# Optimization experiments

Measured on AMD Instinct MI355X. Metric: run time of the kernel, lower is better.

The kernel has to match this reference:

```python
import jax, jax.numpy as jnp
import numpy as np

# Complete 4-ary tree, leaves at depth 8, heap layout (children of i are 4i+1..4i+4).
B_ARY = 4
DEPTH = 8          # depths 0..8, leaves at depth 8
H = 512            # hidden_channels
IN = 512           # in_channels
OUT = 256          # out_channels
L = 2              # num_layers
LEVEL_STARTS = np.array([(B_ARY ** d - 1) // (B_ARY - 1) for d in range(DEPTH + 2)])
N = int(LEVEL_STARTS[-1])  # 87381


def setup_inputs() -> dict:
    key = jax.random.key(0)
    ks = jax.random.split(key, 12)
    x = jax.random.normal(ks[0], (N, IN), jnp.float32)

    # tree structure (numpy, deterministic)
    n_internal = int(LEVEL_STARTS[DEPTH])
    child_idx = np.zeros((N, B_ARY), np.int32)
    child_mask = np.zeros((N, B_ARY), np.int32)
    internal = np.arange(n_internal)
    child_idx[:n_internal] = (internal[:, None] * B_ARY + 1 + np.arange(B_ARY)[None, :]).astype(np.int32)
    child_mask[:n_internal] = 1
    node_parent = np.full(N, -1, np.int64)
    node_parent[1:] = (np.arange(1, N) - 1) // B_ARY
    node_depth = np.zeros(N, np.int64)
    for d in range(DEPTH + 1):
        node_depth[LEVEL_STARTS[d]:LEVEL_STARTS[d + 1]] = d
    is_leaf = node_depth == DEPTH
    edge_index = np.stack([np.arange(1, N), node_parent[1:]]).astype(np.int64)
    batch = np.zeros(N, np.int64)

    s = 0.02
    params = dict(
        W_in=jax.random.normal(ks[1], (IN, H), jnp.float32) * s,
        b_in=jnp.zeros((H,), jnp.float32),
        W_ioux=jax.random.normal(ks[2], (L, H, 3 * H), jnp.float32) * s,
        b_ioux=jnp.zeros((L, 3 * H), jnp.float32),
        W_iouh=jax.random.normal(ks[3], (L, H, 3 * H), jnp.float32) * s,
        b_iouh=jnp.zeros((L, 3 * H), jnp.float32),
        W_fx=jax.random.normal(ks[4], (L, H, H), jnp.float32) * s,
        b_fx=jnp.zeros((L, H), jnp.float32),
        W_fh=jax.random.normal(ks[5], (L, H, H), jnp.float32) * s,
        b_fh=jnp.zeros((L, H), jnp.float32),
        W_out=jax.random.normal(ks[6], (H, OUT), jnp.float32) * s,
        b_out=jnp.zeros((OUT,), jnp.float32),
    )
    return dict(
        x=x,
        edge_index=jnp.asarray(edge_index),
        batch=jnp.asarray(batch),
        node_depth=jnp.asarray(node_depth),
        node_parent=jnp.asarray(node_parent),
        is_leaf=jnp.asarray(is_leaf),
        child_idx=jnp.asarray(child_idx),
        child_mask=jnp.asarray(child_mask),
        **params,
    )


def reference(x, edge_index, batch, node_depth, node_parent, is_leaf,
              child_idx, child_mask,
              W_in, b_in, W_ioux, b_ioux, W_iouh, b_iouh,
              W_fx, b_fx, W_fh, b_fh, W_out, b_out):
    cm = child_mask.astype(x.dtype)  # [N, B]
    h = jax.nn.relu(x @ W_in + b_in)  # input projection (dropout = eval mode identity)
    for l in range(L):
        hidden = jnp.zeros((N, H), x.dtype)
        cell = jnp.zeros((N, H), x.dtype)
        # bottom-up over tree levels; levels are contiguous static slices
        for d in range(DEPTH, -1, -1):
            s, e = int(LEVEL_STARTS[d]), int(LEVEL_STARTS[d + 1])
            xl = h[s:e]                                   # [n_d, H]
            ci = child_idx[s:e]                           # [n_d, B]
            m = cm[s:e][..., None]                        # [n_d, B, 1]
            ch = hidden[ci] * m                           # masked child hidden
            cc = cell[ci] * m                             # masked child cell
            h_sum = ch.sum(axis=1)                        # child-sum
            iou = xl @ W_ioux[l] + b_ioux[l] + h_sum @ W_iouh[l] + b_iouh[l]
            i, o, u = jnp.split(iou, 3, axis=-1)
            i = jax.nn.sigmoid(i)
            o = jax.nn.sigmoid(o)
            u = jnp.tanh(u)
            f = jax.nn.sigmoid((xl @ W_fx[l] + b_fx[l])[:, None, :] + ch @ W_fh[l] + b_fh[l])
            c = i * u + (f * cc).sum(axis=1)
            hl = o * jnp.tanh(c)
            hidden = hidden.at[s:e].set(hl)
            cell = cell.at[s:e].set(c)
        h = hidden
    node_emb = h @ W_out + b_out                          # [N, OUT]
    tree_emb = jax.ops.segment_sum(node_emb, batch, num_segments=1)  # 'sum' aggregation
    return node_emb, tree_emb
```

## Files before the change

### kernel.cpp

```cpp
#include <hip/hip_runtime.h>

typedef __bf16 bf16;
typedef __bf16 bf16x8 __attribute__((ext_vector_type(8)));
typedef float f32x4 __attribute__((ext_vector_type(4)));

#define NN 87381
#define NINT 21845
#define NLEAF 65536
#define LEAF_START 21845

__device__ __forceinline__ float sigmoidf_(float x) {
    return 1.0f / (1.0f + __expf(-x));
}
__device__ __forceinline__ float tanhf_(float x) {
    return 1.0f - 2.0f / (__expf(2.0f * x) + 1.0f);
}

__device__ __forceinline__ void gload_lds16(const bf16* g, bf16* l) {
    __builtin_amdgcn_global_load_lds(
        (const __attribute__((address_space(1))) unsigned int*)g,
        (__attribute__((address_space(3))) unsigned int*)l, 16, 0, 0);
}

__device__ __forceinline__ int xcd_swz(int bid, int nwg) {
    int q = nwg >> 3, r = nwg & 7;
    int x = bid & 7, i = bid >> 3;
    return (x < r ? x * (q + 1) : r * (q + 1) + (x - r) * q) + i;
}

#define SWZ(r, kc) ((((r) << 3) | ((kc) ^ ((r) & 7))) << 3)

__global__ void tconv_kernel(const float* __restrict__ W, bf16* __restrict__ Wt,
                             int NR, int total) {
    int idx = blockIdx.x * 256 + threadIdx.x;
    if (idx >= total) return;
    int n = idx >> 9;
    int k = idx & 511;
    Wt[idx] = (bf16)W[(size_t)k * NR + n];
}

__global__ void tcat_kernel(const float* __restrict__ W1, const float* __restrict__ W2,
                            bf16* __restrict__ Wt, int NR, int total) {
    int idx = blockIdx.x * 256 + threadIdx.x;
    if (idx >= total) return;
    int n = idx >> 10;
    int kk = idx & 1023;
    const float* src = (kk < 512) ? W1 : W2;
    int k = kk & 511;
    Wt[idx] = (bf16)src[(size_t)k * NR + n];
}

__global__ void convx_kernel(const float* __restrict__ X, bf16* __restrict__ Y, int total4) {
    int idx = blockIdx.x * 256 + threadIdx.x;
    if (idx >= total4) return;
    const float4 f = *reinterpret_cast<const float4*>(X + (size_t)idx * 4);
    bf16 o[4] = {(bf16)f.x, (bf16)f.y, (bf16)f.z, (bf16)f.w};
    *reinterpret_cast<ushort2*>(Y + (size_t)idx * 4 + 0) = *reinterpret_cast<ushort2*>(&o[0]);
    *reinterpret_cast<ushort2*>(Y + (size_t)idx * 4 + 2) = *reinterpret_cast<ushort2*>(&o[2]);
}

__global__ void hs_kernel(const bf16* __restrict__ hc, bf16* __restrict__ hs, int total8)
{
    int idx = blockIdx.x * 256 + threadIdx.x;
    if (idx >= total8) return;
    int p  = idx >> 6;
    int j0 = (idx & 63) << 3;
    const bf16* base = hc + ((size_t)(4 * p) << 9) + j0;
    float a8[8];
#pragma unroll
    for (int t = 0; t < 8; ++t) a8[t] = 0.f;
#pragma unroll
    for (int k = 0; k < 4; ++k) {
        const bf16x8 v = *reinterpret_cast<const bf16x8*>(base + (k << 9));
#pragma unroll
        for (int t = 0; t < 8; ++t) a8[t] += (float)v[t];
    }
    bf16x8 o;
#pragma unroll
    for (int t = 0; t < 8; ++t) o[t] = (bf16)a8[t];
    *reinterpret_cast<bf16x8*>(&hs[(size_t)idx * 8]) = o;
}

#define MFMA_COMPUTE_2x4(As, Bs, acc, wm, wn, lm, quad)                          \
    _Pragma("unroll")                                                            \
    for (int kk = 0; kk < 64; kk += 32) {                                        \
        const int kc_ = (kk >> 3) + quad;                                        \
        bf16x8 areg[2], breg[4];                                                 \
        _Pragma("unroll")                                                        \
        for (int mi = 0; mi < 2; ++mi)                                           \
            areg[mi] = *reinterpret_cast<const bf16x8*>(                         \
                &(As)[SWZ(wm + mi * 16 + lm, kc_)]);                             \
        _Pragma("unroll")                                                        \
        for (int ni = 0; ni < 4; ++ni)                                           \
            breg[ni] = *reinterpret_cast<const bf16x8*>(                         \
                &(Bs)[SWZ(wn + ni * 16 + lm, kc_)]);                             \
        _Pragma("unroll")                                                        \
        for (int mi = 0; mi < 2; ++mi)                                           \
            _Pragma("unroll")                                                    \
            for (int ni = 0; ni < 4; ++ni)                                       \
                acc[mi][ni] = __builtin_amdgcn_mfma_f32_16x16x32_bf16(           \
                    areg[mi], breg[ni], acc[mi][ni], 0, 0, 0);                   \
    }

__global__ __launch_bounds__(512)
void gemm_kernel(const bf16* __restrict__ A, const bf16* __restrict__ Bt,
                 int bstride, int K, int ntiles,
                 float* __restrict__ Cf, bf16* __restrict__ Cb,
                 const float* __restrict__ bias1, const float* __restrict__ bias2,
                 int M, int N, int relu, int swz)
{
    __shared__ __align__(16) bf16 As[2][128 * 64];
    __shared__ __align__(16) bf16 Bs[2][128 * 64];
    const int tid  = threadIdx.x;
    const int wave = tid >> 6;
    const int lane = tid & 63;
    int bid = blockIdx.x;
    if (swz) bid = xcd_swz(bid, (int)gridDim.x);
    const int bm = (bid / ntiles) * 128;
    const int bn = (bid % ntiles) * 128;
    const int wm = (wave & 3) * 32;
    const int wn = (wave >> 2) * 64;
    const int lm   = lane & 15;
    const int quad = lane >> 4;

    f32x4 acc[2][4];
#pragma unroll
    for (int i = 0; i < 2; ++i)
#pragma unroll
        for (int j = 0; j < 4; ++j) acc[i][j] = (f32x4){0.f, 0.f, 0.f, 0.f};

    auto stage = [&](int buf, int k0) {
#pragma unroll
        for (int i = 0; i < 2; ++i) {
            int c   = i * 512 + tid;
            int r   = c >> 3;
            int kc8 = ((c & 7) ^ (r & 7)) << 3;
            int gr  = bm + r; gr = (gr < M) ? gr : (M - 1);
            gload_lds16(A + (size_t)gr * K + k0 + kc8, &As[buf][c << 3]);
        }
#pragma unroll
        for (int i = 0; i < 2; ++i) {
            int c   = i * 512 + tid;
            int r   = c >> 3;
            int kc8 = ((c & 7) ^ (r & 7)) << 3;
            gload_lds16(Bt + (size_t)(bn + r) * bstride + k0 + kc8, &Bs[buf][c << 3]);
        }
    };

    const int nk = K >> 6;
    stage(0, 0);
    __syncthreads();
    int cur = 0;
    for (int t = 0; t < nk; ++t) {
        if (t + 1 < nk) stage(cur ^ 1, (t + 1) << 6);
        MFMA_COMPUTE_2x4(As[cur], Bs[cur], acc, wm, wn, lm, quad);
        __syncthreads();
        cur ^= 1;
    }

#pragma unroll
    for (int ni = 0; ni < 4; ++ni) {
        int col = bn + wn + ni * 16 + lm;
        float bsum = (bias1 ? bias1[col] : 0.f) + (bias2 ? bias2[col] : 0.f);
#pragma unroll
        for (int mi = 0; mi < 2; ++mi) {
#pragma unroll
            for (int r = 0; r < 4; ++r) {
                int row = bm + wm + mi * 16 + quad * 4 + r;
                if (row < M) {
                    float v = acc[mi][ni][r] + bsum;
                    if (relu) v = (v > 0.f) ? v : 0.f;
                    if (Cf) Cf[(size_t)row * N + col] = v;
                    else    Cb[(size_t)row * N + col] = (bf16)v;
                }
            }
        }
    }
}

__global__ __launch_bounds__(512)
void iou_fused_kernel(const bf16* __restrict__ A0, const bf16* __restrict__ A1,
                      int K, const bf16* __restrict__ wiou,
                      const float* __restrict__ bx1, const float* __restrict__ bx2,
                      const float* __restrict__ fcs,
                      bf16* __restrict__ hout, float* __restrict__ cellout,
                      int M, int swz)
{
    __shared__ __align__(16) bf16 As[2][128 * 64];
    __shared__ __align__(16) bf16 Bs[2][3 * 64 * 64];
    const int tid  = threadIdx.x;
    const int wave = tid >> 6;
    const int lane = tid & 63;
    int bid = blockIdx.x;
    if (swz) bid = xcd_swz(bid, (int)gridDim.x);
    const int bm = (bid >> 3) * 128;
    const int bn = (bid & 7) * 64;
    if (bm >= M) return;
    const int wm   = (wave & 3) * 32;
    const int wn   = (wave >> 2) * 32;
    const int lm   = lane & 15;
    const int quad = lane >> 4;

    f32x4 acc[3][2][2];
#pragma unroll
    for (int g = 0; g < 3; ++g)
#pragma unroll
        for (int i = 0; i < 2; ++i)
#pragma unroll
            for (int j = 0; j < 2; ++j) acc[g][i][j] = (f32x4){0.f, 0.f, 0.f, 0.f};

    auto stage = [&](int buf, int k0) {
        const bf16* Aseg = (k0 < 512) ? A0 : A1;
        const int kseg0 = k0 & 511;
#pragma unroll
        for (int i = 0; i < 2; ++i) {
            int c   = i * 512 + tid;
            int r   = c >> 3;
            int kc8 = ((c & 7) ^ (r & 7)) << 3;
            int gr  = bm + r; gr = (gr < M) ? gr : (M - 1);
            gload_lds16(Aseg + ((size_t)gr << 9) + kseg0 + kc8, &As[buf][c << 3]);
        }
#pragma unroll
        for (int i = 0; i < 3; ++i) {
            int c   = i * 512 + tid;
            int g   = c >> 9;
            int cg  = c & 511;
            int r   = cg >> 3;
            int kc8 = ((cg & 7) ^ (r & 7)) << 3;
            gload_lds16(wiou + (size_t)(g * 512 + bn + r) * 1024 + k0 + kc8,
                        &Bs[buf][c << 3]);
        }
    };

    const int nk = K >> 6;
    stage(0, 0);
    __syncthreads();
    int cur = 0;
    for (int t = 0; t < nk; ++t) {
        if (t + 1 < nk) stage(cur ^ 1, (t + 1) << 6);
#pragma unroll
        for (int kk = 0; kk < 64; kk += 32) {
            const int kc_ = (kk >> 3) + quad;
            bf16x8 areg[2];
#pragma unroll
            for (int mi = 0; mi < 2; ++mi)
                areg[mi] = *reinterpret_cast<const bf16x8*>(
                    &As[cur][SWZ(wm + mi * 16 + lm, kc_)]);
            bf16x8 breg[3][2];
#pragma unroll
            for (int g = 0; g < 3; ++g)
#pragma unroll
                for (int ni = 0; ni < 2; ++ni)
                    breg[g][ni] = *reinterpret_cast<const bf16x8*>(
                        &Bs[cur][g * 4096 + SWZ(wn + ni * 16 + lm, kc_)]);
#pragma unroll
            for (int g = 0; g < 3; ++g)
#pragma unroll
                for (int mi = 0; mi < 2; ++mi)
#pragma unroll
                    for (int ni = 0; ni < 2; ++ni)
                        acc[g][mi][ni] = __builtin_amdgcn_mfma_f32_16x16x32_bf16(
                            areg[mi], breg[g][ni], acc[g][mi][ni], 0, 0, 0);
        }
        __syncthreads();
        cur ^= 1;
    }

#pragma unroll
    for (int ni = 0; ni < 2; ++ni) {
        int col = bn + wn + ni * 16 + lm;
        float bi = bx1[col]        + bx2[col];
        float bo = bx1[col + 512]  + bx2[col + 512];
        float bu = bx1[col + 1024] + bx2[col + 1024];
#pragma unroll
        for (int mi = 0; mi < 2; ++mi) {
#pragma unroll
            for (int r = 0; r < 4; ++r) {
                int row = bm + wm + mi * 16 + quad * 4 + r;
                if (row < M) {
                    float i_ = sigmoidf_(acc[0][mi][ni][r] + bi);
                    float o_ = sigmoidf_(acc[1][mi][ni][r] + bo);
                    float u_ = tanhf_(acc[2][mi][ni][r] + bu);
                    float c  = i_ * u_ + (fcs ? fcs[(size_t)row * 512 + col] : 0.f);
                    cellout[(size_t)row * 512 + col] = c;
                    hout[(size_t)row * 512 + col] = (bf16)(o_ * tanhf_(c));
                }
            }
        }
    }
}

__global__ __launch_bounds__(512)
void cf_kernel(const bf16* __restrict__ hp, const bf16* __restrict__ hc,
               const float* __restrict__ cellc, const bf16* __restrict__ wf,
               const float* __restrict__ bf1, const float* __restrict__ bf2,
               float* __restrict__ fcs, int E, int swz)
{
    const int M = 4 * E;
    __shared__ __align__(16) bf16 As[2][128 * 64];
    __shared__ __align__(16) bf16 Bs[2][128 * 64];
    const int tid  = threadIdx.x;
    const int wave = tid >> 6;
    const int lane = tid & 63;
    int bid = blockIdx.x;
    if (swz) bid = xcd_swz(bid, (int)gridDim.x);
    const int bm = (bid >> 2) * 128;
    const int bn = (bid & 3) * 128;
    if (bm >= M) return;
    const int wm   = (wave & 3) * 32;
    const int wn   = (wave >> 2) * 64;
    const int lm   = lane & 15;
    const int quad = lane >> 4;

    f32x4 acc[2][4];
#pragma unroll
    for (int i = 0; i < 2; ++i)
#pragma unroll
        for (int j = 0; j < 4; ++j) acc[i][j] = (f32x4){0.f, 0.f, 0.f, 0.f};

    auto stage = [&](int buf, int k0) {
        const int seg   = k0 >> 9;
        const int kseg0 = k0 & 511;
#pragma unroll
        for (int i = 0; i < 2; ++i) {
            int c   = i * 512 + tid;
            int r   = c >> 3;
            int kc8 = ((c & 7) ^ (r & 7)) << 3;
            int gr  = bm + r; gr = (gr < M) ? gr : (M - 1);
            const bf16* src = (seg == 0) ? (hp + ((size_t)(gr >> 2) << 9))
                                         : (hc + ((size_t)gr << 9));
            gload_lds16(src + kseg0 + kc8, &As[buf][c << 3]);
        }
#pragma unroll
        for (int i = 0; i < 2; ++i) {
            int c   = i * 512 + tid;
            int r   = c >> 3;
            int kc8 = ((c & 7) ^ (r & 7)) << 3;
            gload_lds16(wf + (size_t)(bn + r) * 1024 + k0 + kc8, &Bs[buf][c << 3]);
        }
    };

    stage(0, 0);
    __syncthreads();
    int cur = 0;
    for (int t = 0; t < 16; ++t) {
        if (t + 1 < 16) stage(cur ^ 1, (t + 1) << 6);
        MFMA_COMPUTE_2x4(As[cur], Bs[cur], acc, wm, wn, lm, quad);
        __syncthreads();
        cur ^= 1;
    }

#pragma unroll
    for (int ni = 0; ni < 4; ++ni) {
        int col = bn + wn + ni * 16 + lm;
        float bsum = bf1[col] + bf2[col];
#pragma unroll
        for (int mi = 0; mi < 2; ++mi) {
            int R0 = bm + wm + mi * 16;
            if (R0 + quad * 4 < M) {
                float fc = 0.f;
#pragma unroll
                for (int r = 0; r < 4; ++r) {
                    int row = R0 + quad * 4 + r;
                    fc += sigmoidf_(acc[mi][ni][r] + bsum) *
                          cellc[(size_t)row * 512 + col];
                }
                fcs[(size_t)((R0 >> 2) + quad) * 512 + col] = fc;
            }
        }
    }
}

#define R1_BLOCKS 2048
#define R1_ROWS 43
__global__ void reduce1_kernel(const float* __restrict__ ne, float* __restrict__ partial)
{
    int t = threadIdx.x;
    int b = blockIdx.x;
    int r0 = b * R1_ROWS;
    int r1 = r0 + R1_ROWS; r1 = (r1 < NN) ? r1 : NN;
    float acc = 0.f;
    for (int r = r0; r < r1; ++r) acc += ne[(size_t)r * 256 + t];
    partial[(size_t)b * 256 + t] = acc;
}
__global__ void reduce2_kernel(const float* __restrict__ partial, float* __restrict__ partial2)
{
    int t = threadIdx.x;
    int b = blockIdx.x;
    float acc = 0.f;
    for (int i = 0; i < 32; ++i) acc += partial[(size_t)(b * 32 + i) * 256 + t];
    partial2[(size_t)b * 256 + t] = acc;
}
__global__ void reduce3_kernel(const float* __restrict__ partial2, float* __restrict__ tree)
{
    int t = threadIdx.x;
    float acc = 0.f;
    for (int i = 0; i < 64; ++i) acc += partial2[(size_t)i * 256 + t];
    tree[t] = acc;
}

extern "C" void kernel_launch(void* const* d_in, const int* in_sizes, int n_in,
                              void* d_out, int out_size, void* d_ws, size_t ws_size,
                              hipStream_t stream)
{
    const float* x      = (const float*)d_in[0];
    const float* W_in   = (const float*)d_in[8];
    const float* b_in   = (const float*)d_in[9];
    const float* W_ioux = (const float*)d_in[10];
    const float* b_ioux = (const float*)d_in[11];
    const float* W_iouh = (const float*)d_in[12];
    const float* b_iouh = (const float*)d_in[13];
    const float* W_fx   = (const float*)d_in[14];
    const float* b_fx   = (const float*)d_in[15];
    const float* W_fh   = (const float*)d_in[16];
    const float* b_fh   = (const float*)d_in[17];
    const float* W_out  = (const float*)d_in[18];
    const float* b_out  = (const float*)d_in[19];

    static const int LS[10] = {0, 1, 5, 21, 85, 341, 1365, 5461, 21845, 87381};

    char* ws = (char*)d_ws;
    size_t off = 0;
    auto take = [&](size_t bytes) -> void* {
        void* p = ws + off;
        off += (bytes + 255) & ~(size_t)255;
        return p;
    };
    bf16*  wt_in      = (bf16*) take((size_t)512 * 512 * 2);
    bf16*  wt_out     = (bf16*) take((size_t)256 * 512 * 2);
    bf16*  wt_iou_cat = (bf16*) take((size_t)2 * 1536 * 1024 * 2);
    bf16*  wt_f_cat   = (bf16*) take((size_t)2 * 512 * 1024 * 2);
    bf16*  h          = (bf16*) take((size_t)NN * 512 * 2);
    bf16*  hint1      = (bf16*) take((size_t)NINT * 512 * 2);
    bf16*  hB         = (bf16*) take((size_t)NLEAF * 512 * 2);
    float* cell_int   = (float*)take((size_t)NINT * 512 * 4);
    float* cell_leaf  = (float*)take((size_t)NLEAF * 512 * 4);
    float* fcsum      = (float*)take((size_t)16384 * 512 * 4);
    bf16*  hsbuf      = (bf16*) take((size_t)16384 * 512 * 2);
    float* partial    = (float*)take((size_t)R1_BLOCKS * 256 * 4);
    float* partial2   = (float*)take((size_t)64 * 256 * 4);
    bf16*  xbf        = (bf16*)cell_leaf;

    dim3 blk(256), blk512(512);
    auto tgrid = [](int total) { return dim3((unsigned)((total + 255) / 256)); };

    tconv_kernel<<<tgrid(512 * 512), blk, 0, stream>>>(W_in, wt_in, 512, 512 * 512);
    tconv_kernel<<<tgrid(256 * 512), blk, 0, stream>>>(W_out, wt_out, 256, 256 * 512);
    for (int l = 0; l < 2; ++l) {
        tcat_kernel<<<tgrid(1536 * 1024), blk, 0, stream>>>(
            W_ioux + (size_t)l * 512 * 1536, W_iouh + (size_t)l * 512 * 1536,
            wt_iou_cat + (size_t)l * 1536 * 1024, 1536, 1536 * 1024);
        tcat_kernel<<<tgrid(512 * 1024), blk, 0, stream>>>(
            W_fx + (size_t)l * 512 * 512, W_fh + (size_t)l * 512 * 512,
            wt_f_cat + (size_t)l * 512 * 1024, 512, 512 * 1024);
    }

    auto gemm = [&](const bf16* A, const bf16* Bt, int bstride, int K,
                    float* Cf, bf16* Cb, const float* b1, const float* b2,
                    int M, int N, int relu, int swz) {
        int mt = (M + 127) / 128, nt = N / 128;
        gemm_kernel<<<dim3((unsigned)(mt * nt)), blk512, 0, stream>>>(
            A, Bt, bstride, K, nt, Cf, Cb, b1, b2, M, N, relu, swz);
    };

    convx_kernel<<<tgrid(NN * 128), blk, 0, stream>>>(x, xbf, NN * 128);
    gemm(xbf, wt_in, 512, 512, nullptr, h, b_in, nullptr, NN, 512, 1, 1);

    for (int l = 0; l < 2; ++l) {
        const bf16* wiou = wt_iou_cat + (size_t)l * 1536 * 1024;
        const bf16* wf   = wt_f_cat + (size_t)l * 512 * 1024;
        const float* bx1 = b_ioux + (size_t)l * 1536;
        const float* bx2 = b_iouh + (size_t)l * 1536;
        const float* bf1 = b_fx + (size_t)l * 512;
        const float* bf2 = b_fh + (size_t)l * 512;

        const bf16* lin   = (l == 0) ? (h + (size_t)LEAF_START * 512) : hB;
        bf16*       lout  = (l == 0) ? hB : (h + (size_t)LEAF_START * 512);
        const bf16* hprev = (l == 0) ? h : hint1;
        bf16*       hcur  = (l == 0) ? hint1 : h;

        {
            int mt = NLEAF / 128;
            iou_fused_kernel<<<dim3((unsigned)(mt * 8)), blk512, 0, stream>>>(
                lin, nullptr, 512, wiou, bx1, bx2, nullptr,
                lout, cell_leaf, NLEAF, 1);
        }

        for (int d = 7; d >= 0; --d) {
            int s  = LS[d];
            int E  = LS[d + 1] - LS[d];
            int cs = LS[d + 1];
            const bf16*  hc = (d == 7) ? lout : (hcur + (size_t)cs * 512);
            const float* cc = (d == 7) ? cell_leaf : (cell_int + (size_t)cs * 512);

            hs_kernel<<<tgrid(E * 64), blk, 0, stream>>>(hc, hsbuf, E * 64);

            int mt_cf = (4 * E + 127) / 128;
            cf_kernel<<<dim3((unsigned)(mt_cf * 4)), blk512, 0, stream>>>(
                hprev + (size_t)s * 512, hc, cc, wf, bf1, bf2, fcsum, E, 1);

            int mt_iou = (E + 127) / 128;
            iou_fused_kernel<<<dim3((unsigned)(mt_iou * 8)), blk512, 0, stream>>>(
                hprev + (size_t)s * 512, hsbuf, 1024, wiou, bx1, bx2, fcsum,
                hcur + (size_t)s * 512, cell_int + (size_t)s * 512, E, 1);
        }
    }

    float* node_emb = (float*)d_out;
    gemm(h, wt_out, 512, 512, node_emb, nullptr, b_out, nullptr, NN, 256, 0, 1);
    reduce1_kernel<<<dim3(R1_BLOCKS), blk, 0, stream>>>(node_emb, partial);
    reduce2_kernel<<<dim3(64), blk, 0, stream>>>(partial, partial2);
    reduce3_kernel<<<dim3(1), blk, 0, stream>>>(partial2, node_emb + (size_t)NN * 256);
}
```

Baseline: 1.849 ms.

## Fuse child hidden-sum into IOU epilogue, store cell in bf16, precompute load pointers

The separate hs_kernel pass is removed. The IOU kernel epilogue now sums each group of four consecutive child rows in registers and writes the parent's child-sum into ping-pong buffers for the next level. Cell state is stored as bf16 instead of fp32, which halves its memory traffic and lowers precision. The GEMM staging lambdas precompute per-thread global pointers and LDS offsets so each stage does less address arithmetic. The fused sum is taken over bf16-rounded h and assumes a 128-row tile holds whole groups of four children.

After: 1.717 ms. 7.2% less time.

```diff
diff --git a/kernel.cpp b/kernel.cpp
--- a/kernel.cpp
+++ b/kernel.cpp
@@ -57,28 +57,6 @@
     bf16 o[4] = {(bf16)f.x, (bf16)f.y, (bf16)f.z, (bf16)f.w};
     *reinterpret_cast<ushort2*>(Y + (size_t)idx * 4 + 0) = *reinterpret_cast<ushort2*>(&o[0]);
     *reinterpret_cast<ushort2*>(Y + (size_t)idx * 4 + 2) = *reinterpret_cast<ushort2*>(&o[2]);
-}
-
-__global__ void hs_kernel(const bf16* __restrict__ hc, bf16* __restrict__ hs, int total8)
-{
-    int idx = blockIdx.x * 256 + threadIdx.x;
-    if (idx >= total8) return;
-    int p  = idx >> 6;
-    int j0 = (idx & 63) << 3;
-    const bf16* base = hc + ((size_t)(4 * p) << 9) + j0;
-    float a8[8];
-#pragma unroll
-    for (int t = 0; t < 8; ++t) a8[t] = 0.f;
-#pragma unroll
-    for (int k = 0; k < 4; ++k) {
-        const bf16x8 v = *reinterpret_cast<const bf16x8*>(base + (k << 9));
-#pragma unroll
-        for (int t = 0; t < 8; ++t) a8[t] += (float)v[t];
-    }
-    bf16x8 o;
-#pragma unroll
-    for (int t = 0; t < 8; ++t) o[t] = (bf16)a8[t];
-    *reinterpret_cast<bf16x8*>(&hs[(size_t)idx * 8]) = o;
 }
 
 #define MFMA_COMPUTE_2x4(As, Bs, acc, wm, wn, lm, quad)                          \
@@ -129,22 +107,28 @@
 #pragma unroll
         for (int j = 0; j < 4; ++j) acc[i][j] = (f32x4){0.f, 0.f, 0.f, 0.f};
 
-    auto stage = [&](int buf, int k0) {
-#pragma unroll
-        for (int i = 0; i < 2; ++i) {
-            int c   = i * 512 + tid;
-            int r   = c >> 3;
-            int kc8 = ((c & 7) ^ (r & 7)) << 3;
-            int gr  = bm + r; gr = (gr < M) ? gr : (M - 1);
-            gload_lds16(A + (size_t)gr * K + k0 + kc8, &As[buf][c << 3]);
-        }
-#pragma unroll
-        for (int i = 0; i < 2; ++i) {
-            int c   = i * 512 + tid;
-            int r   = c >> 3;
-            int kc8 = ((c & 7) ^ (r & 7)) << 3;
-            gload_lds16(Bt + (size_t)(bn + r) * bstride + k0 + kc8, &Bs[buf][c << 3]);
-        }
+    const bf16* aptr[2];
+    const bf16* bptr[2];
+    int loff[2];
+#pragma unroll
+    for (int i = 0; i < 2; ++i) {
+        int c   = i * 512 + tid;
+        int r   = c >> 3;
+        int kc8 = ((c & 7) ^ (r & 7)) << 3;
+        int gr  = bm + r; gr = (gr < M) ? gr : (M - 1);
+        aptr[i] = A + (size_t)gr * K + kc8;
+        bptr[i] = Bt + (size_t)(bn + r) * bstride + kc8;
+        loff[i] = c << 3;
+    }
+
+    auto stage = [&](int buf, int t) {
+        const int kofs = t << 6;
+#pragma unroll
+        for (int i = 0; i < 2; ++i)
+            gload_lds16(aptr[i] + kofs, &As[0][0] + buf * (128 * 64) + loff[i]);
+#pragma unroll
+        for (int i = 0; i < 2; ++i)
+            gload_lds16(bptr[i] + kofs, &Bs[0][0] + buf * (128 * 64) + loff[i]);
     };
 
     const int nk = K >> 6;
@@ -152,7 +136,7 @@
     __syncthreads();
     int cur = 0;
     for (int t = 0; t < nk; ++t) {
-        if (t + 1 < nk) stage(cur ^ 1, (t + 1) << 6);
+        if (t + 1 < nk) stage(cur ^ 1, t + 1);
         MFMA_COMPUTE_2x4(As[cur], Bs[cur], acc, wm, wn, lm, quad);
         __syncthreads();
         cur ^= 1;
@@ -183,7 +167,8 @@
                       int K, const bf16* __restrict__ wiou,
                       const float* __restrict__ bx1, const float* __restrict__ bx2,
                       const float* __restrict__ fcs,
-                      bf16* __restrict__ hout, float* __restrict__ cellout,
+                      bf16* __restrict__ hout, bf16* __restrict__ cellout,
+                      bf16* __restrict__ hsout,
                       int M, int swz)
 {
     __shared__ __align__(16) bf16 As[2][128 * 64];
@@ -209,27 +194,44 @@
 #pragma unroll
             for (int j = 0; j < 2; ++j) acc[g][i][j] = (f32x4){0.f, 0.f, 0.f, 0.f};
 
-    auto stage = [&](int buf, int k0) {
-        const bf16* Aseg = (k0 < 512) ? A0 : A1;
-        const int kseg0 = k0 & 511;
+    const bf16* A1s = A1 ? A1 : A0;
+    const bf16* aptr0[2];
+    const bf16* aptr1[2];
+    int aoff[2];
+#pragma unroll
+    for (int i = 0; i < 2; ++i) {
+        int c   = i * 512 + tid;
+        int r   = c >> 3;
+        int kc8 = ((c & 7) ^ (r & 7)) << 3;
+        int gr  = bm + r; gr = (gr < M) ? gr : (M - 1);
+        aptr0[i] = A0  + ((size_t)gr << 9) + kc8;
+        aptr1[i] = A1s + ((size_t)gr << 9) + kc8;
+        aoff[i]  = c << 3;
+    }
+    const bf16* bptr[3];
+    int boff[3];
+#pragma unroll
+    for (int i = 0; i < 3; ++i) {
+        int c   = i * 512 + tid;
+        int g   = c >> 9;
+        int cg  = c & 511;
+        int r   = cg >> 3;
+        int kc8 = ((cg & 7) ^ (r & 7)) << 3;
+        bptr[i] = wiou + (size_t)(g * 512 + bn + r) * 1024 + kc8;
+        boff[i] = c << 3;
+    }
+
+    auto stage = [&](int buf, int t) {
+        const int kofs = (t & 7) << 6;
 #pragma unroll
         for (int i = 0; i < 2; ++i) {
-            int c   = i * 512 + tid;
-            int r   = c >> 3;
-            int kc8 = ((c & 7) ^ (r & 7)) << 3;
-            int gr  = bm + r; gr = (gr < M) ? gr : (M - 1);
-            gload_lds16(Aseg + ((size_t)gr << 9) + kseg0 + kc8, &As[buf][c << 3]);
-        }
-#pragma unroll
-        for (int i = 0; i < 3; ++i) {
-            int c   = i * 512 + tid;
-            int g   = c >> 9;
-            int cg  = c & 511;
-            int r   = cg >> 3;
-            int kc8 = ((cg & 7) ^ (r & 7)) << 3;
-            gload_lds16(wiou + (size_t)(g * 512 + bn + r) * 1024 + k0 + kc8,
-                        &Bs[buf][c << 3]);
-        }
+            const bf16* g = ((t < 8) ? aptr0[i] : aptr1[i]) + kofs;
+            gload_lds16(g, &As[0][0] + buf * (128 * 64) + aoff[i]);
+        }
+        const int bofs = t << 6;
+#pragma unroll
+        for (int i = 0; i < 3; ++i)
+            gload_lds16(bptr[i] + bofs, &Bs[0][0] + buf * (3 * 64 * 64) + boff[i]);
     };
 
     const int nk = K >> 6;
@@ -237,7 +239,7 @@
     __syncthreads();
     int cur = 0;
     for (int t = 0; t < nk; ++t) {
-        if (t + 1 < nk) stage(cur ^ 1, (t + 1) << 6);
+        if (t + 1 < nk) stage(cur ^ 1, t + 1);
 #pragma unroll
         for (int kk = 0; kk < 64; kk += 32) {
             const int kc_ = (kk >> 3) + quad;
@@ -274,25 +276,31 @@
         float bu = bx1[col + 1024] + bx2[col + 1024];
 #pragma unroll
         for (int mi = 0; mi < 2; ++mi) {
+            int rbase = bm + wm + mi * 16 + quad * 4;
+            float hsum = 0.f;
 #pragma unroll
             for (int r = 0; r < 4; ++r) {
-                int row = bm + wm + mi * 16 + quad * 4 + r;
+                int row = rbase + r;
                 if (row < M) {
                     float i_ = sigmoidf_(acc[0][mi][ni][r] + bi);
                     float o_ = sigmoidf_(acc[1][mi][ni][r] + bo);
                     float u_ = tanhf_(acc[2][mi][ni][r] + bu);
                     float c  = i_ * u_ + (fcs ? fcs[(size_t)row * 512 + col] : 0.f);
-                    cellout[(size_t)row * 512 + col] = c;
-                    hout[(size_t)row * 512 + col] = (bf16)(o_ * tanhf_(c));
+                    bf16 hb  = (bf16)(o_ * tanhf_(c));
+                    cellout[(size_t)row * 512 + col] = (bf16)c;
+                    hout[(size_t)row * 512 + col] = hb;
+                    hsum += (float)hb;
                 }
             }
+            if (hsout && rbase < M)
+                hsout[(size_t)(rbase >> 2) * 512 + col] = (bf16)hsum;
         }
     }
 }
 
 __global__ __launch_bounds__(512)
 void cf_kernel(const bf16* __restrict__ hp, const bf16* __restrict__ hc,
-               const float* __restrict__ cellc, const bf16* __restrict__ wf,
+               const bf16* __restrict__ cellc, const bf16* __restrict__ wf,
                const float* __restrict__ bf1, const float* __restrict__ bf2,
                float* __restrict__ fcs, int E, int swz)
 {
@@ -318,33 +326,40 @@
 #pragma unroll
         for (int j = 0; j < 4; ++j) acc[i][j] = (f32x4){0.f, 0.f, 0.f, 0.f};
 
-    auto stage = [&](int buf, int k0) {
-        const int seg   = k0 >> 9;
-        const int kseg0 = k0 & 511;
+    const bf16* aptrP[2];
+    const bf16* aptrC[2];
+    const bf16* bptr[2];
+    int loff[2];
+#pragma unroll
+    for (int i = 0; i < 2; ++i) {
+        int c   = i * 512 + tid;
+        int r   = c >> 3;
+        int kc8 = ((c & 7) ^ (r & 7)) << 3;
+        int gr  = bm + r; gr = (gr < M) ? gr : (M - 1);
+        aptrP[i] = hp + ((size_t)(gr >> 2) << 9) + kc8;
+        aptrC[i] = hc + ((size_t)gr << 9) + kc8;
+        bptr[i]  = wf + (size_t)(bn + r) * 1024 + kc8;
+        loff[i]  = c << 3;
+    }
+
+    auto stage = [&](int buf, int t) {
+        const int kofs = (t & 7) << 6;
 #pragma unroll
         for (int i = 0; i < 2; ++i) {
-            int c   = i * 512 + tid;
-            int r   = c >> 3;
-            int kc8 = ((c & 7) ^ (r & 7)) << 3;
-            int gr  = bm + r; gr = (gr < M) ? gr : (M - 1);
-            const bf16* src = (seg == 0) ? (hp + ((size_t)(gr >> 2) << 9))
-                                         : (hc + ((size_t)gr << 9));
-            gload_lds16(src + kseg0 + kc8, &As[buf][c << 3]);
-        }
-#pragma unroll
-        for (int i = 0; i < 2; ++i) {
-            int c   = i * 512 + tid;
-            int r   = c >> 3;
-            int kc8 = ((c & 7) ^ (r & 7)) << 3;
-            gload_lds16(wf + (size_t)(bn + r) * 1024 + k0 + kc8, &Bs[buf][c << 3]);
-        }
+            const bf16* g = ((t < 8) ? aptrP[i] : aptrC[i]) + kofs;
+            gload_lds16(g, &As[0][0] + buf * (128 * 64) + loff[i]);
+        }
+        const int bofs = t << 6;
+#pragma unroll
+        for (int i = 0; i < 2; ++i)
+            gload_lds16(bptr[i] + bofs, &Bs[0][0] + buf * (128 * 64) + loff[i]);
     };
 
     stage(0, 0);
     __syncthreads();
     int cur = 0;
     for (int t = 0; t < 16; ++t) {
-        if (t + 1 < 16) stage(cur ^ 1, (t + 1) << 6);
+        if (t + 1 < 16) stage(cur ^ 1, t + 1);
         MFMA_COMPUTE_2x4(As[cur], Bs[cur], acc, wm, wn, lm, quad);
         __syncthreads();
         cur ^= 1;
@@ -363,7 +378,7 @@
                 for (int r = 0; r < 4; ++r) {
                     int row = R0 + quad * 4 + r;
                     fc += sigmoidf_(acc[mi][ni][r] + bsum) *
-                          cellc[(size_t)row * 512 + col];
+                          (float)cellc[(size_t)row * 512 + col];
                 }
                 fcs[(size_t)((R0 >> 2) + quad) * 512 + col] = fc;
             }
@@ -433,13 +448,14 @@
     bf16*  h          = (bf16*) take((size_t)NN * 512 * 2);
     bf16*  hint1      = (bf16*) take((size_t)NINT * 512 * 2);
     bf16*  hB         = (bf16*) take((size_t)NLEAF * 512 * 2);
-    float* cell_int   = (float*)take((size_t)NINT * 512 * 4);
-    float* cell_leaf  = (float*)take((size_t)NLEAF * 512 * 4);
+    bf16*  cell_int   = (bf16*) take((size_t)NINT * 512 * 2);
+    bf16*  cell_leaf  = (bf16*) take((size_t)NLEAF * 512 * 2);
     float* fcsum      = (float*)take((size_t)16384 * 512 * 4);
-    bf16*  hsbuf      = (bf16*) take((size_t)16384 * 512 * 2);
+    bf16*  hsA        = (bf16*) take((size_t)16384 * 512 * 2);
+    bf16*  hsB        = (bf16*) take((size_t)4096 * 512 * 2);
     float* partial    = (float*)take((size_t)R1_BLOCKS * 256 * 4);
     float* partial2   = (float*)take((size_t)64 * 256 * 4);
-    bf16*  xbf        = (bf16*)cell_leaf;
+    bf16*  xbf        = cell_int;
 
     dim3 blk(256), blk512(512);
     auto tgrid = [](int total) { return dim3((unsigned)((total + 255) / 256)); };
@@ -483,17 +499,17 @@
             int mt = NLEAF / 128;
             iou_fused_kernel<<<dim3((unsigned)(mt * 8)), blk512, 0, stream>>>(
                 lin, nullptr, 512, wiou, bx1, bx2, nullptr,
-                lout, cell_leaf, NLEAF, 1);
+                lout, cell_leaf, hsA, NLEAF, 1);
         }
 
         for (int d = 7; d >= 0; --d) {
             int s  = LS[d];
             int E  = LS[d + 1] - LS[d];
             int cs = LS[d + 1];
-            const bf16*  hc = (d == 7) ? lout : (hcur + (size_t)cs * 512);
-            const float* cc = (d == 7) ? cell_leaf : (cell_int + (size_t)cs * 512);
-
-            hs_kernel<<<tgrid(E * 64), blk, 0, stream>>>(hc, hsbuf, E * 64);
+            const bf16* hc = (d == 7) ? lout : (hcur + (size_t)cs * 512);
+            const bf16* cc = (d == 7) ? cell_leaf : (cell_int + (size_t)cs * 512);
+            bf16* hs_read  = (d & 1) ? hsA : hsB;
+            bf16* hs_write = (d == 0) ? nullptr : ((d & 1) ? hsB : hsA);
 
             int mt_cf = (4 * E + 127) / 128;
             cf_kernel<<<dim3((unsigned)(mt_cf * 4)), blk512, 0, stream>>>(
@@ -501,8 +517,8 @@
 
             int mt_iou = (E + 127) / 128;
             iou_fused_kernel<<<dim3((unsigned)(mt_iou * 8)), blk512, 0, stream>>>(
-                hprev + (size_t)s * 512, hsbuf, 1024, wiou, bx1, bx2, fcsum,
-                hcur + (size_t)s * 512, cell_int + (size_t)s * 512, E, 1);
+                hprev + (size_t)s * 512, hs_read, 1024, wiou, bx1, bx2, fcsum,
+                hcur + (size_t)s * 512, cell_int + (size_t)s * 512, hs_write, E, 1);
         }
     }
 
```
